# Kernel optimization log

Measured on AMD Instinct MI355X. Metric: run time of the kernel, lower is better.

The kernel has to match this reference:

```python
import jax, jax.numpy as jnp
import numpy as np

BATCH, SEQ, D_MODEL, D_STATE = 8, 4096, 128, 128


def setup_inputs() -> dict:
    key = jax.random.key(0)
    ks = jax.random.split(key, 6)
    x = jax.random.normal(ks[0], (BATCH, SEQ, D_MODEL), jnp.float32)
    # Stable (negative) eigenvalues so A_discrete = exp(dt*Lambda) < 1 and powers don't overflow.
    Lam = -(jax.random.uniform(ks[1], (D_STATE,), jnp.float32) * 2.0 + 0.1)
    B = jax.random.normal(ks[2], (D_STATE, D_MODEL), jnp.float32) / np.sqrt(D_STATE)
    C = jax.random.normal(ks[3], (D_MODEL, D_STATE), jnp.float32) / np.sqrt(D_STATE)
    Dv = jax.random.normal(ks[4], (D_MODEL,), jnp.float32)
    log_dt = (jax.random.uniform(ks[5], (D_MODEL,), jnp.float32)
              * (np.log(0.001) - np.log(0.1)) + np.log(0.1)).astype(jnp.float32)
    return {"x": x, "Lam": Lam, "B": B, "C": C, "Dv": Dv, "log_dt": log_dt}


def _s4_forward(x, Lam, B, C, Dv, log_dt):
    # x: (batch, L, M) with transposed=False
    _, L, M = x.shape
    dt = jnp.exp(log_dt)                                    # (M,)
    rate = dt[:, None] * Lam[None, :]                       # (M, N) = log(A_discrete)
    ell = jnp.arange(L, dtype=x.dtype)                      # (L,)
    # powers[m, s, l] = A_discrete[m, s] ** l  (closed form of the sequential cumprod)
    powers = jnp.exp(rate[:, :, None] * ell[None, None, :])  # (M, N, L)
    # Original: einsum('ds,msl->dsl', B, powers) sums over m, giving B[d,s]*Psum[s,l];
    # then einsum('md,dsl->ml', C, .) contracts d and s -> kernel = C @ B @ Psum.
    Psum = powers.sum(axis=0)                               # (N, L)
    kernel = C @ (B @ Psum)                                 # (M, L)
    xt = jnp.transpose(x, (0, 2, 1))                        # (B, M, L)
    n = 2 * L  # zero-padded linear convolution via FFT
    y_fft = jnp.fft.rfft(xt, n=n) * jnp.fft.rfft(kernel, n=n)[None]
    y = jnp.fft.irfft(y_fft, n=n)[..., :L]                  # (B, M, L)
    y = y + Dv[None, :, None] * xt                          # skip connection D*u
    return jnp.transpose(y, (0, 2, 1))                      # (B, L, M)


def reference(x, Lam, B, C, Dv, log_dt):
    return _s4_forward(x, Lam, B, C, Dv, log_dt)
```

## Files before the change

### kernel.cpp

```cpp
#include <hip/hip_runtime.h>
#include <math.h>

#define BATCH 8
#define SEQ   4096
#define DM    128
#define DS    128
#define NFFT  8192
#define NT    512
#define NTP   256
#define NBUT  (NFFT / 4)
#define PERT  (NBUT / NT)

__device__ __forceinline__ float2 cmulf(float2 a, float2 b) {
    return make_float2(a.x * b.x - a.y * b.y, a.x * b.y + a.y * b.x);
}
__device__ __forceinline__ float2 caddf(float2 a, float2 b) { return make_float2(a.x + b.x, a.y + b.y); }
__device__ __forceinline__ float2 csubf(float2 a, float2 b) { return make_float2(a.x - b.x, a.y - b.y); }


__global__ void prep_G(const float* __restrict__ Cm, const float* __restrict__ Bm,
                       float* __restrict__ G) {
    int gid = blockIdx.x * blockDim.x + threadIdx.x;
    int m = gid >> 7, j = gid & 127;
    float acc = 0.f;
    for (int i = 0; i < DS; ++i) acc += Cm[m * DS + i] * Bm[i * DM + j];
    G[gid] = acc;
}

__global__ void prep_psum(const float* __restrict__ Lam, const float* __restrict__ logdt,
                          float* __restrict__ Psum) {
    __shared__ float sdt[DM];
    int tid = threadIdx.x;
    if (tid < DM) sdt[tid] = __expf(logdt[tid]);
    __syncthreads();
    int s = blockIdx.x;
    int l = blockIdx.y * NTP + tid;
    float t = Lam[s] * (float)l;
    float acc = 0.f;
    for (int m = 0; m < DM; ++m) acc += __expf(sdt[m] * t);
    Psum[s * SEQ + l] = acc;
}

__global__ void prep_K(const float* __restrict__ G, const float* __restrict__ Psum,
                       float* __restrict__ K) {
    int m = blockIdx.y;
    int l = blockIdx.x * NTP + threadIdx.x;
    float acc = 0.f;
    for (int s = 0; s < DS; ++s) acc += G[m * DS + s] * Psum[s * SEQ + l];
    K[m * SEQ + l] = acc;
}


__device__ __forceinline__ void r4_fwd(float2* z, int tid, int q) {
    const float astep = -(float)M_PI / (2.0f * (float)q);
#pragma unroll
    for (int k = 0; k < PERT; ++k) {
        int idx = tid + k * NT;
        int j = idx & (q - 1);
        int base = ((idx & ~(q - 1)) << 2) | j;
        float2 a0 = z[base], a1 = z[base + q], a2 = z[base + 2 * q], a3 = z[base + 3 * q];
        float sn, cs; __sincosf(astep * (float)j, &sn, &cs);
        float2 w1 = make_float2(cs, sn);
        float2 w2 = cmulf(w1, w1);
        float2 w3 = cmulf(w1, w2);
        float2 t0 = caddf(a0, a2), t1 = csubf(a0, a2);
        float2 t2 = caddf(a1, a3), t3 = csubf(a1, a3);
        z[base]         = caddf(t0, t2);
        z[base + q]     = cmulf(make_float2(t1.x + t3.y, t1.y - t3.x), w1);
        z[base + 2 * q] = cmulf(csubf(t0, t2), w2);
        z[base + 3 * q] = cmulf(make_float2(t1.x - t3.y, t1.y + t3.x), w3);
    }
}

__device__ __forceinline__ void r4_inv(float2* z, int tid, int q) {
    const float astep = (float)M_PI / (2.0f * (float)q);
#pragma unroll
    for (int k = 0; k < PERT; ++k) {
        int idx = tid + k * NT;
        int j = idx & (q - 1);
        int base = ((idx & ~(q - 1)) << 2) | j;
        float2 y0 = z[base], y1 = z[base + q], y2 = z[base + 2 * q], y3 = z[base + 3 * q];
        float sn, cs; __sincosf(astep * (float)j, &sn, &cs);
        float2 w1 = make_float2(cs, sn);
        float2 w2 = cmulf(w1, w1);
        float2 w3 = cmulf(w1, w2);
        float2 b1 = cmulf(y1, w1), b2 = cmulf(y2, w2), b3 = cmulf(y3, w3);
        float2 t0 = caddf(y0, b2), t2 = csubf(y0, b2);
        float2 t1 = caddf(b1, b3);
        float2 t3 = make_float2(-(b1.y - b3.y), b1.x - b3.x);
        z[base]         = caddf(t0, t1);
        z[base + 2 * q] = csubf(t0, t1);
        z[base + q]     = caddf(t2, t3);
        z[base + 3 * q] = csubf(t2, t3);
    }
}


__global__ void __launch_bounds__(NT, 4) fft_K(const float* __restrict__ K,
                                               float2* __restrict__ Kf) {
    __shared__ __align__(16) float2 z[NFFT];
    int tid = threadIdx.x, m = blockIdx.x;

    {
        const float astep = -(float)M_PI / 4096.0f;
#pragma unroll
        for (int k = 0; k < PERT; ++k) {
            int j = tid + k * NT;
            float a0 = K[m * SEQ + j];
            float a1 = K[m * SEQ + j + 2048];
            float sn, cs; __sincosf(astep * (float)j, &sn, &cs);
            float2 w1 = make_float2(cs, sn);
            float2 w2 = cmulf(w1, w1);
            float2 w3 = cmulf(w1, w2);
            z[j]        = make_float2(a0 + a1, 0.f);
            z[j + 2048] = cmulf(make_float2(a0, -a1), w1);
            z[j + 4096] = cmulf(make_float2(a0 - a1, 0.f), w2);
            z[j + 6144] = cmulf(make_float2(a0,  a1), w3);
        }
    }
    __syncthreads();
    r4_fwd(z, tid, 512); __syncthreads();
    r4_fwd(z, tid, 128); __syncthreads();
    r4_fwd(z, tid, 32);  __syncthreads();
    r4_fwd(z, tid, 8);   __syncthreads();
    r4_fwd(z, tid, 2);   __syncthreads();
    {
        const float4* z4 = (const float4*)z;
        float4* kf4 = (float4*)(Kf + (size_t)m * NFFT);
#pragma unroll
        for (int k = 0; k < NFFT / 2 / NT; ++k) {
            int i = tid + k * NT;
            float4 p = z4[i];
            kf4[i] = make_float4(p.x + p.z, p.y + p.w, p.x - p.z, p.y - p.w);
        }
    }
}


__global__ void transpose_xin(const float* __restrict__ x, float* __restrict__ xt) {
    __shared__ float tile[32][33];
    int b = blockIdx.z;
    int l0 = blockIdx.x * 32, m0 = blockIdx.y * 32;
    int tx = threadIdx.x, ty = threadIdx.y;
    for (int r = 0; r < 4; ++r) {
        int l = l0 + ty + r * 8;
        tile[ty + r * 8][tx] = x[(size_t)b * SEQ * DM + (size_t)l * DM + m0 + tx];
    }
    __syncthreads();
    for (int r = 0; r < 4; ++r) {
        int m = m0 + ty + r * 8;
        xt[(size_t)b * DM * SEQ + (size_t)m * SEQ + l0 + tx] = tile[tx][ty + r * 8];
    }
}

__global__ void transpose_yout(const float* __restrict__ yt, float* __restrict__ out) {
    __shared__ float tile[32][33];
    int b = blockIdx.z;
    int l0 = blockIdx.x * 32, m0 = blockIdx.y * 32;
    int tx = threadIdx.x, ty = threadIdx.y;
    for (int r = 0; r < 4; ++r) {
        int m = m0 + ty + r * 8;
        tile[ty + r * 8][tx] = yt[(size_t)b * DM * SEQ + (size_t)m * SEQ + l0 + tx];
    }
    __syncthreads();
    for (int r = 0; r < 4; ++r) {
        int l = l0 + ty + r * 8;
        out[(size_t)b * SEQ * DM + (size_t)l * DM + m0 + tx] = tile[tx][ty + r * 8];
    }
}


__global__ void __launch_bounds__(NT, 4) conv_fft(float* __restrict__ xt,
                                                  const float2* __restrict__ Kf,
                                                  const float* __restrict__ Dv) {
    __shared__ __align__(16) float2 z[NFFT];
    int tid = threadIdx.x;
    int m  = blockIdx.x & (DM - 1);
    int bp = blockIdx.x >> 7;
    size_t base0 = ((size_t)(2 * bp) * DM + m) * SEQ;
    size_t base1 = ((size_t)(2 * bp + 1) * DM + m) * SEQ;

    {
        const float astep = -(float)M_PI / 4096.0f;
#pragma unroll
        for (int k = 0; k < PERT; ++k) {
            int j = tid + k * NT;
            float2 a0 = make_float2(xt[base0 + j],        xt[base1 + j]);
            float2 a1 = make_float2(xt[base0 + j + 2048], xt[base1 + j + 2048]);
            float sn, cs; __sincosf(astep * (float)j, &sn, &cs);
            float2 w1 = make_float2(cs, sn);
            float2 w2 = cmulf(w1, w1);
            float2 w3 = cmulf(w1, w2);
            z[j]        = caddf(a0, a1);
            z[j + 2048] = cmulf(make_float2(a0.x + a1.y, a0.y - a1.x), w1);
            z[j + 4096] = cmulf(csubf(a0, a1), w2);
            z[j + 6144] = cmulf(make_float2(a0.x - a1.y, a0.y + a1.x), w3);
        }
    }
    __syncthreads();
    r4_fwd(z, tid, 512); __syncthreads();
    r4_fwd(z, tid, 128); __syncthreads();
    r4_fwd(z, tid, 32);  __syncthreads();
    r4_fwd(z, tid, 8);   __syncthreads();
    r4_fwd(z, tid, 2);   __syncthreads();

    {
        float4* z4 = (float4*)z;
        const float4* kf4 = (const float4*)(Kf + (size_t)m * NFFT);
#pragma unroll
        for (int k = 0; k < NFFT / 2 / NT; ++k) {
            int i = tid + k * NT;
            float4 p = z4[i];
            float2 u0 = make_float2(p.x + p.z, p.y + p.w);
            float2 u1 = make_float2(p.x - p.z, p.y - p.w);
            float4 kk = kf4[i];
            u0 = cmulf(u0, make_float2(kk.x, kk.y));
            u1 = cmulf(u1, make_float2(kk.z, kk.w));
            z4[i] = make_float4(u0.x + u1.x, u0.y + u1.y, u0.x - u1.x, u0.y - u1.y);
        }
    }
    __syncthreads();
    r4_inv(z, tid, 2);   __syncthreads();
    r4_inv(z, tid, 8);   __syncthreads();
    r4_inv(z, tid, 32);  __syncthreads();
    r4_inv(z, tid, 128); __syncthreads();
    r4_inv(z, tid, 512); __syncthreads();

    {
        const float astep = (float)M_PI / 4096.0f;
        const float invN = 1.0f / (float)NFFT;
        float dv = Dv[m];
#pragma unroll
        for (int k = 0; k < PERT; ++k) {
            int j = tid + k * NT;
            float2 y0 = z[j], y1 = z[j + 2048], y2 = z[j + 4096], y3 = z[j + 6144];
            float sn, cs; __sincosf(astep * (float)j, &sn, &cs);
            float2 w1 = make_float2(cs, sn);
            float2 w2 = cmulf(w1, w1);
            float2 w3 = cmulf(w1, w2);
            float2 b1 = cmulf(y1, w1), b2 = cmulf(y2, w2), b3 = cmulf(y3, w3);
            float2 t0 = caddf(y0, b2), t2 = csubf(y0, b2);
            float2 t1 = caddf(b1, b3);
            float2 t3 = make_float2(-(b1.y - b3.y), b1.x - b3.x);
            float2 r0 = caddf(t0, t1);
            float2 r1 = caddf(t2, t3);
            float x00 = xt[base0 + j],        x10 = xt[base1 + j];
            float x01 = xt[base0 + j + 2048], x11 = xt[base1 + j + 2048];
            xt[base0 + j]        = r0.x * invN + dv * x00;
            xt[base1 + j]        = r0.y * invN + dv * x10;
            xt[base0 + j + 2048] = r1.x * invN + dv * x01;
            xt[base1 + j + 2048] = r1.y * invN + dv * x11;
        }
    }
}

extern "C" void kernel_launch(void* const* d_in, const int* in_sizes, int n_in,
                              void* d_out, int out_size, void* d_ws, size_t ws_size,
                              hipStream_t stream) {
    const float* x     = (const float*)d_in[0];
    const float* Lam   = (const float*)d_in[1];
    const float* Bm    = (const float*)d_in[2];
    const float* Cm    = (const float*)d_in[3];
    const float* Dv    = (const float*)d_in[4];
    const float* logdt = (const float*)d_in[5];
    float* out = (float*)d_out;

    float*  ws   = (float*)d_ws;
    float*  xt   = ws;
    float2* Kf   = (float2*)(ws + 4194304);
    float*  K    = ws + 4194304 + 2097152;
    float*  Psum = K + 524288;
    float*  G    = Psum + 524288;

    hipLaunchKernelGGL(prep_G,         dim3(64),         dim3(NTP),    0, stream, Cm, Bm, G);
    hipLaunchKernelGGL(prep_psum,      dim3(128, 16),    dim3(NTP),    0, stream, Lam, logdt, Psum);
    hipLaunchKernelGGL(prep_K,         dim3(16, 128),    dim3(NTP),    0, stream, G, Psum, K);
    hipLaunchKernelGGL(fft_K,          dim3(128),        dim3(NT),     0, stream, K, Kf);
    hipLaunchKernelGGL(transpose_xin,  dim3(128, 4, 8),  dim3(32, 8),  0, stream, x, xt);
    hipLaunchKernelGGL(conv_fft,       dim3(512),        dim3(NT),     0, stream, xt, Kf, Dv);
    hipLaunchKernelGGL(transpose_yout, dim3(128, 4, 8),  dim3(32, 8),  0, stream, xt, out);
}
```

Before: 147.7 us.

## Replace paired complex FFT convolution with real-to-complex half-size FFT using precomputed PQ filters

The convolution no longer packs two batches into one 8192-point complex FFT. It treats each real length-8192 padded sequence as a 4096-point complex FFT of even/odd pairs. The real-FFT split/merge and the kernel spectrum multiply are folded into precomputed per-frequency P/Q coefficients, applied in place on bit-reversed indices, so no separate spectral post-processing pass is needed. This halves shared memory per block to 32KB with 256 threads, doubles the block count, and adds a prep_PQ kernel and a larger workspace. It relies on the implicit zero-padding of the upper half of the input and on correct bit-reversed index pairing.

```diff
diff --git a/kernel.cpp b/kernel.cpp
--- a/kernel.cpp
+++ b/kernel.cpp
@@ -5,17 +5,25 @@
 #define SEQ   4096
 #define DM    128
 #define DS    128
-#define NFFT  8192
-#define NT    512
+#define N2    4096
+#define NT    256
 #define NTP   256
-#define NBUT  (NFFT / 4)
-#define PERT  (NBUT / NT)
+#define NPAIR 2048
+#define KFS   4100
+#define PERT  4
 
 __device__ __forceinline__ float2 cmulf(float2 a, float2 b) {
     return make_float2(a.x * b.x - a.y * b.y, a.x * b.y + a.y * b.x);
 }
 __device__ __forceinline__ float2 caddf(float2 a, float2 b) { return make_float2(a.x + b.x, a.y + b.y); }
 __device__ __forceinline__ float2 csubf(float2 a, float2 b) { return make_float2(a.x - b.x, a.y - b.y); }
+__device__ __forceinline__ float2 conjf2(float2 a) { return make_float2(a.x, -a.y); }
+__device__ __forceinline__ float2 cisf(float t) { float s, c; __sincosf(t, &s, &c); return make_float2(c, s); }
+
+__device__ __forceinline__ int dr12(int i) {
+    unsigned br = __brev((unsigned)i) >> 20;
+    return (int)(((br & 0x555u) << 1) | ((br >> 1) & 0x555u));
+}
 
 
 __global__ void prep_G(const float* __restrict__ Cm, const float* __restrict__ Bm,
@@ -59,8 +67,7 @@
         int j = idx & (q - 1);
         int base = ((idx & ~(q - 1)) << 2) | j;
         float2 a0 = z[base], a1 = z[base + q], a2 = z[base + 2 * q], a3 = z[base + 3 * q];
-        float sn, cs; __sincosf(astep * (float)j, &sn, &cs);
-        float2 w1 = make_float2(cs, sn);
+        float2 w1 = cisf(astep * (float)j);
         float2 w2 = cmulf(w1, w1);
         float2 w3 = cmulf(w1, w2);
         float2 t0 = caddf(a0, a2), t1 = csubf(a0, a2);
@@ -80,8 +87,7 @@
         int j = idx & (q - 1);
         int base = ((idx & ~(q - 1)) << 2) | j;
         float2 y0 = z[base], y1 = z[base + q], y2 = z[base + 2 * q], y3 = z[base + 3 * q];
-        float sn, cs; __sincosf(astep * (float)j, &sn, &cs);
-        float2 w1 = make_float2(cs, sn);
+        float2 w1 = cisf(astep * (float)j);
         float2 w2 = cmulf(w1, w1);
         float2 w3 = cmulf(w1, w2);
         float2 b1 = cmulf(y1, w1), b2 = cmulf(y2, w2), b3 = cmulf(y3, w3);
@@ -95,44 +101,119 @@
     }
 }
 
-
-__global__ void __launch_bounds__(NT, 4) fft_K(const float* __restrict__ K,
-                                               float2* __restrict__ Kf) {
-    __shared__ __align__(16) float2 z[NFFT];
+__device__ __forceinline__ void fwd_first_fused(float2* z, const float2* __restrict__ vrow, int tid) {
+    const float astep = -(float)M_PI / 2048.0f;
+#pragma unroll
+    for (int c = 0; c < PERT; ++c) {
+        int n = tid + c * NT;
+        float2 a0 = vrow[n];
+        float2 a1 = vrow[n + 1024];
+        float2 w1 = cisf(astep * (float)n);
+        float2 w2 = cmulf(w1, w1);
+        float2 w3 = cmulf(w1, w2);
+        z[n]        = caddf(a0, a1);
+        z[n + 1024] = cmulf(make_float2(a0.x + a1.y, a0.y - a1.x), w1);
+        z[n + 2048] = cmulf(csubf(a0, a1), w2);
+        z[n + 3072] = cmulf(make_float2(a0.x - a1.y, a0.y + a1.x), w3);
+    }
+}
+
+
+__global__ void __launch_bounds__(NT, 4) fft_Kf(const float* __restrict__ K,
+                                                float2* __restrict__ Kf) {
+    __shared__ __align__(16) float2 z[N2];
     int tid = threadIdx.x, m = blockIdx.x;
-
-    {
-        const float astep = -(float)M_PI / 4096.0f;
-#pragma unroll
-        for (int k = 0; k < PERT; ++k) {
-            int j = tid + k * NT;
-            float a0 = K[m * SEQ + j];
-            float a1 = K[m * SEQ + j + 2048];
-            float sn, cs; __sincosf(astep * (float)j, &sn, &cs);
-            float2 w1 = make_float2(cs, sn);
-            float2 w2 = cmulf(w1, w1);
-            float2 w3 = cmulf(w1, w2);
-            z[j]        = make_float2(a0 + a1, 0.f);
-            z[j + 2048] = cmulf(make_float2(a0, -a1), w1);
-            z[j + 4096] = cmulf(make_float2(a0 - a1, 0.f), w2);
-            z[j + 6144] = cmulf(make_float2(a0,  a1), w3);
+    const float2* krow = (const float2*)(K + (size_t)m * SEQ);
+
+    fwd_first_fused(z, krow, tid);
+    __syncthreads();
+    r4_fwd(z, tid, 256); __syncthreads();
+    r4_fwd(z, tid, 64);  __syncthreads();
+    r4_fwd(z, tid, 16);  __syncthreads();
+    r4_fwd(z, tid, 4);   __syncthreads();
+    r4_fwd(z, tid, 1);   __syncthreads();
+
+    float2* out = Kf + (size_t)m * KFS;
+#pragma unroll
+    for (int c = 0; c < 8; ++c) {
+        int pp = tid + c * NT;
+        if (pp == 0) {
+            float2 v0 = z[0];
+            out[0]    = make_float2(v0.x + v0.y, 0.f);
+            out[4096] = make_float2(v0.x - v0.y, 0.f);
+            float2 v2 = z[2];
+            out[2048] = conjf2(v2);
+        } else {
+            int i  = ((pp >> 1) << 2) | (pp & 1);
+            int k  = dr12(i);
+            int kp = 4096 - k;
+            int ip = dr12(kp);
+            float2 va = z[i], vb = z[ip];
+            float2 e  = cisf(-(float)M_PI * (float)k / 4096.0f);
+            float2 cb = conjf2(vb);
+            float2 s  = caddf(va, cb), d = csubf(va, cb);
+            float2 pr = cmulf(e, d);
+            out[k] = make_float2(0.5f * (s.x + pr.y), 0.5f * (s.y - pr.x));
+            float2 ep = make_float2(-e.x, e.y);
+            float2 ca = conjf2(va);
+            float2 s2 = caddf(vb, ca), d2 = csubf(vb, ca);
+            float2 p2 = cmulf(ep, d2);
+            out[kp] = make_float2(0.5f * (s2.x + p2.y), 0.5f * (s2.y - p2.x));
         }
     }
-    __syncthreads();
-    r4_fwd(z, tid, 512); __syncthreads();
-    r4_fwd(z, tid, 128); __syncthreads();
-    r4_fwd(z, tid, 32);  __syncthreads();
-    r4_fwd(z, tid, 8);   __syncthreads();
-    r4_fwd(z, tid, 2);   __syncthreads();
-    {
-        const float4* z4 = (const float4*)z;
-        float4* kf4 = (float4*)(Kf + (size_t)m * NFFT);
-#pragma unroll
-        for (int k = 0; k < NFFT / 2 / NT; ++k) {
-            int i = tid + k * NT;
-            float4 p = z4[i];
-            kf4[i] = make_float4(p.x + p.z, p.y + p.w, p.x - p.z, p.y - p.w);
-        }
+}
+
+
+__device__ __forceinline__ void pq_one(float2 Kk, float2 Kkp, float thk,
+                                       float2 fap, float2 fbp,
+                                       float2* P, float2* Q) {
+    float2 e  = cisf(-thk);
+    float2 fa = make_float2(0.5f * (1.f + e.y), -0.5f * e.x);
+    float2 fb = make_float2(0.5f * (1.f - e.y),  0.5f * e.x);
+    float2 ak = cmulf(Kk, fa), bk = cmulf(Kk, fb);
+    float2 apv = cmulf(Kkp, fap), bpv = cmulf(Kkp, fbp);
+    float2 g = make_float2(0.5f * (1.f + e.y), 0.5f * e.x);
+    float2 h = make_float2(0.5f * (1.f - e.y), -0.5f * e.x);
+    *P = caddf(cmulf(g, ak), cmulf(h, conjf2(bpv)));
+    *Q = caddf(cmulf(g, bk), cmulf(h, conjf2(apv)));
+}
+
+__device__ __forceinline__ void pq_pair(float2 Kk, float2 Kkp, float thk, float thkp,
+                                        float2* Pk, float2* Qk, float2* Pkp, float2* Qkp) {
+    float2 e  = cisf(-thk);
+    float2 ep = cisf(-thkp);
+    float2 fa  = make_float2(0.5f * (1.f + e.y),  -0.5f * e.x);
+    float2 fb  = make_float2(0.5f * (1.f - e.y),   0.5f * e.x);
+    float2 fap = make_float2(0.5f * (1.f + ep.y), -0.5f * ep.x);
+    float2 fbp = make_float2(0.5f * (1.f - ep.y),  0.5f * ep.x);
+    pq_one(Kk,  Kkp, thk,  fap, fbp, Pk,  Qk);
+    pq_one(Kkp, Kk,  thkp, fa,  fb,  Pkp, Qkp);
+}
+
+__global__ void prep_PQ(const float2* __restrict__ Kf, float4* __restrict__ PQ) {
+    int m = blockIdx.x;
+    int p = blockIdx.y * NTP + threadIdx.x;
+    const float2* kf = Kf + (size_t)m * KFS;
+    float4* dst = PQ + ((size_t)m * NPAIR + p) * 2;
+    float2 Pk, Qk, Pkp, Qkp;
+    if (p == 0) {
+        float2 P0, Q0, Pd, Qd;
+        pq_pair(kf[0], kf[4096], 0.f, (float)M_PI, &P0, &Q0, &Pd, &Qd);
+        float th2 = (float)M_PI * 0.5f;
+        float2 P2, Q2, Pd2, Qd2;
+        pq_pair(kf[2048], kf[2048], th2, th2, &P2, &Q2, &Pd2, &Qd2);
+        dst[0] = make_float4(P0.x, P0.y, Q0.x, Q0.y);
+        dst[1] = make_float4(P2.x, P2.y, Q2.x, Q2.y);
+    } else {
+        int i  = ((p >> 1) << 2) | (p & 1);
+        int k  = dr12(i);
+        int kp = 4096 - k;
+        pq_pair(kf[k], kf[kp],
+                (float)M_PI * (float)k / 4096.0f,
+                (float)M_PI * (float)kp / 4096.0f,
+                &Pk, &Qk, &Pkp, &Qkp);
+        dst[0] = make_float4(Pk.x, Pk.y, Qk.x, Qk.y);
+        dst[1] = make_float4(Pkp.x, Pkp.y, Qkp.x, Qkp.y);
     }
 }
 
@@ -170,72 +251,67 @@
 }
 
 
-__global__ void __launch_bounds__(NT, 4) conv_fft(float* __restrict__ xt,
-                                                  const float2* __restrict__ Kf,
+__global__ void __launch_bounds__(NT, 5) conv_r2c(float* __restrict__ xt,
+                                                  const float4* __restrict__ PQ,
                                                   const float* __restrict__ Dv) {
-    __shared__ __align__(16) float2 z[NFFT];
+    __shared__ __align__(16) float2 z[N2];
     int tid = threadIdx.x;
-    int m  = blockIdx.x & (DM - 1);
-    int bp = blockIdx.x >> 7;
-    size_t base0 = ((size_t)(2 * bp) * DM + m) * SEQ;
-    size_t base1 = ((size_t)(2 * bp + 1) * DM + m) * SEQ;
+    int m = blockIdx.x & (DM - 1);
+    int b = blockIdx.x >> 7;
+    float2* xrow = (float2*)(xt + (((size_t)b * DM + m) << 12));
+
+    fwd_first_fused(z, xrow, tid);
+    __syncthreads();
+    r4_fwd(z, tid, 256); __syncthreads();
+    r4_fwd(z, tid, 64);  __syncthreads();
+    r4_fwd(z, tid, 16);  __syncthreads();
+    r4_fwd(z, tid, 4);   __syncthreads();
+    r4_fwd(z, tid, 1);   __syncthreads();
 
     {
-        const float astep = -(float)M_PI / 4096.0f;
-#pragma unroll
-        for (int k = 0; k < PERT; ++k) {
-            int j = tid + k * NT;
-            float2 a0 = make_float2(xt[base0 + j],        xt[base1 + j]);
-            float2 a1 = make_float2(xt[base0 + j + 2048], xt[base1 + j + 2048]);
-            float sn, cs; __sincosf(astep * (float)j, &sn, &cs);
-            float2 w1 = make_float2(cs, sn);
-            float2 w2 = cmulf(w1, w1);
-            float2 w3 = cmulf(w1, w2);
-            z[j]        = caddf(a0, a1);
-            z[j + 2048] = cmulf(make_float2(a0.x + a1.y, a0.y - a1.x), w1);
-            z[j + 4096] = cmulf(csubf(a0, a1), w2);
-            z[j + 6144] = cmulf(make_float2(a0.x - a1.y, a0.y + a1.x), w3);
+        const float4* pq = PQ + (size_t)m * NPAIR * 2;
+#pragma unroll
+        for (int c = 0; c < 8; ++c) {
+            int pp = tid + c * NT;
+            float4 lo = pq[2 * pp];
+            float4 hi = pq[2 * pp + 1];
+            if (pp == 0) {
+                float2 v0 = z[0];
+                z[0] = caddf(cmulf(make_float2(lo.x, lo.y), v0),
+                             cmulf(make_float2(lo.z, lo.w), conjf2(v0)));
+                float2 v2 = z[2];
+                z[2] = caddf(cmulf(make_float2(hi.x, hi.y), v2),
+                             cmulf(make_float2(hi.z, hi.w), conjf2(v2)));
+            } else {
+                int i  = ((pp >> 1) << 2) | (pp & 1);
+                int k  = dr12(i);
+                int kp = 4096 - k;
+                int ip = dr12(kp);
+                float2 va = z[i], vb = z[ip];
+                z[i]  = caddf(cmulf(make_float2(lo.x, lo.y), va),
+                              cmulf(make_float2(lo.z, lo.w), conjf2(vb)));
+                z[ip] = caddf(cmulf(make_float2(hi.x, hi.y), vb),
+                              cmulf(make_float2(hi.z, hi.w), conjf2(va)));
+            }
         }
     }
     __syncthreads();
-    r4_fwd(z, tid, 512); __syncthreads();
-    r4_fwd(z, tid, 128); __syncthreads();
-    r4_fwd(z, tid, 32);  __syncthreads();
-    r4_fwd(z, tid, 8);   __syncthreads();
-    r4_fwd(z, tid, 2);   __syncthreads();
+
+    r4_inv(z, tid, 1);   __syncthreads();
+    r4_inv(z, tid, 4);   __syncthreads();
+    r4_inv(z, tid, 16);  __syncthreads();
+    r4_inv(z, tid, 64);  __syncthreads();
+    r4_inv(z, tid, 256); __syncthreads();
 
     {
-        float4* z4 = (float4*)z;
-        const float4* kf4 = (const float4*)(Kf + (size_t)m * NFFT);
-#pragma unroll
-        for (int k = 0; k < NFFT / 2 / NT; ++k) {
-            int i = tid + k * NT;
-            float4 p = z4[i];
-            float2 u0 = make_float2(p.x + p.z, p.y + p.w);
-            float2 u1 = make_float2(p.x - p.z, p.y - p.w);
-            float4 kk = kf4[i];
-            u0 = cmulf(u0, make_float2(kk.x, kk.y));
-            u1 = cmulf(u1, make_float2(kk.z, kk.w));
-            z4[i] = make_float4(u0.x + u1.x, u0.y + u1.y, u0.x - u1.x, u0.y - u1.y);
-        }
-    }
-    __syncthreads();
-    r4_inv(z, tid, 2);   __syncthreads();
-    r4_inv(z, tid, 8);   __syncthreads();
-    r4_inv(z, tid, 32);  __syncthreads();
-    r4_inv(z, tid, 128); __syncthreads();
-    r4_inv(z, tid, 512); __syncthreads();
-
-    {
-        const float astep = (float)M_PI / 4096.0f;
-        const float invN = 1.0f / (float)NFFT;
+        const float astep = (float)M_PI / 2048.0f;
+        const float invN = 1.0f / 4096.0f;
         float dv = Dv[m];
 #pragma unroll
-        for (int k = 0; k < PERT; ++k) {
-            int j = tid + k * NT;
-            float2 y0 = z[j], y1 = z[j + 2048], y2 = z[j + 4096], y3 = z[j + 6144];
-            float sn, cs; __sincosf(astep * (float)j, &sn, &cs);
-            float2 w1 = make_float2(cs, sn);
+        for (int c = 0; c < PERT; ++c) {
+            int j = tid + c * NT;
+            float2 y0 = z[j], y1 = z[j + 1024], y2 = z[j + 2048], y3 = z[j + 3072];
+            float2 w1 = cisf(astep * (float)j);
             float2 w2 = cmulf(w1, w1);
             float2 w3 = cmulf(w1, w2);
             float2 b1 = cmulf(y1, w1), b2 = cmulf(y2, w2), b3 = cmulf(y3, w3);
@@ -244,12 +320,10 @@
             float2 t3 = make_float2(-(b1.y - b3.y), b1.x - b3.x);
             float2 r0 = caddf(t0, t1);
             float2 r1 = caddf(t2, t3);
-            float x00 = xt[base0 + j],        x10 = xt[base1 + j];
-            float x01 = xt[base0 + j + 2048], x11 = xt[base1 + j + 2048];
-            xt[base0 + j]        = r0.x * invN + dv * x00;
-            xt[base1 + j]        = r0.y * invN + dv * x10;
-            xt[base0 + j + 2048] = r1.x * invN + dv * x01;
-            xt[base1 + j + 2048] = r1.y * invN + dv * x11;
+            float2 x0 = xrow[j];
+            float2 x1 = xrow[j + 1024];
+            xrow[j]        = make_float2(r0.x * invN + dv * x0.x, r0.y * invN + dv * x0.y);
+            xrow[j + 1024] = make_float2(r1.x * invN + dv * x1.x, r1.y * invN + dv * x1.y);
         }
     }
 }
@@ -268,15 +342,17 @@
     float*  ws   = (float*)d_ws;
     float*  xt   = ws;
     float2* Kf   = (float2*)(ws + 4194304);
-    float*  K    = ws + 4194304 + 2097152;
+    float4* PQ   = (float4*)(ws + 4194304 + 1049600);
+    float*  K    = ws + 4194304 + 1049600 + 2097152;
     float*  Psum = K + 524288;
     float*  G    = Psum + 524288;
 
     hipLaunchKernelGGL(prep_G,         dim3(64),         dim3(NTP),    0, stream, Cm, Bm, G);
     hipLaunchKernelGGL(prep_psum,      dim3(128, 16),    dim3(NTP),    0, stream, Lam, logdt, Psum);
     hipLaunchKernelGGL(prep_K,         dim3(16, 128),    dim3(NTP),    0, stream, G, Psum, K);
-    hipLaunchKernelGGL(fft_K,          dim3(128),        dim3(NT),     0, stream, K, Kf);
+    hipLaunchKernelGGL(fft_Kf,         dim3(128),        dim3(NT),     0, stream, K, (float2*)Kf);
+    hipLaunchKernelGGL(prep_PQ,        dim3(128, 8),     dim3(NTP),    0, stream, (const float2*)Kf, PQ);
     hipLaunchKernelGGL(transpose_xin,  dim3(128, 4, 8),  dim3(32, 8),  0, stream, x, xt);
-    hipLaunchKernelGGL(conv_fft,       dim3(512),        dim3(NT),     0, stream, xt, Kf, Dv);
+    hipLaunchKernelGGL(conv_r2c,       dim3(1024),       dim3(NT),     0, stream, xt, (const float4*)PQ, Dv);
     hipLaunchKernelGGL(transpose_yout, dim3(128, 4, 8),  dim3(32, 8),  0, stream, xt, out);
 }
```

After: 151.5 us. +2.6%, slower.
